# Performance work log

Hardware: AMD Instinct MI355X
Metric: run time of the kernel (lower is better)

Reference implementation:

```python
import jax, jax.numpy as jnp
import numpy as np

B, L, DIN = 2048, 70, 15
HID, NF, K = 16, 4, 40          # hidden_units//2, n_features, kernel_size
C = DIN + 1 + NF                # 20 signature input channels (original + time + conv features)
Z0 = 64
SIG_CH = C + C * C + C ** 3     # 8420, depth-3 signature channels


def setup_inputs() -> dict:
    key = jax.random.key(0)
    ks = jax.random.split(key, 8)
    return {
        "observed_data": jax.random.normal(ks[0], (B, L, DIN), jnp.float32),
        "observed_tp": jnp.linspace(0.0, 1.0, L, dtype=jnp.float32),
        "conv1_w": jax.random.normal(ks[1], (HID, DIN, K), jnp.float32) / np.float32(np.sqrt(DIN * K)),
        "conv1_b": jnp.zeros((HID,), jnp.float32),
        "conv2_w": jax.random.normal(ks[2], (HID, HID), jnp.float32) / np.float32(np.sqrt(HID)),
        "conv2_b": jnp.zeros((HID,), jnp.float32),
        "conv3_w": jax.random.normal(ks[3], (NF, HID), jnp.float32) / np.float32(np.sqrt(HID)),
        "conv3_b": jnp.zeros((NF,), jnp.float32),
        "w_out": jax.random.normal(ks[4], (2 * Z0, SIG_CH), jnp.float32) * np.float32(np.sqrt(2.0 / (SIG_CH + 2 * Z0))),
        "b_out": jnp.zeros((2 * Z0,), jnp.float32),
    }


def _augment(x, w1, b1, w2, b2, w3, b3):
    # x: (B, L, DIN).  signatory.Augment: conv(K) -> relu -> conv1x1 -> relu -> conv1x1,
    # then concat [truncated original, time channel, conv features] along channels.
    xc = jnp.transpose(x, (0, 2, 1))                                   # (B, DIN, L)
    h = jax.lax.conv_general_dilated(xc, w1, (1,), 'VALID')            # (B, HID, Lp)
    h = h + b1[None, :, None]
    h = jnp.einsum('oc,bcl->bol', w2, jax.nn.relu(h)) + b2[None, :, None]
    h = jnp.einsum('oc,bcl->bol', w3, jax.nn.relu(h)) + b3[None, :, None]
    conv_out = jnp.transpose(h, (0, 2, 1))                             # (B, Lp, NF)
    Lp = conv_out.shape[1]
    orig = x[:, K - 1:, :]                                             # (B, Lp, DIN)
    t = jnp.linspace(0.0, 1.0, Lp, dtype=x.dtype)
    time = jnp.broadcast_to(t[None, :, None], (x.shape[0], Lp, 1))
    return jnp.concatenate([orig, time, conv_out], axis=2)             # (B, Lp, C)


def _signature_depth3(path):
    # Truncated (depth 3) path signature with basepoint=True, via Chen's identity:
    # S <- S \otimes exp(dx) over increments, zero basepoint prepended.
    incs = jnp.diff(path, axis=1, prepend=jnp.zeros_like(path[:, :1]))  # (B, Lp, C)
    incs = jnp.transpose(incs, (1, 0, 2))                               # (Lp, B, C)
    Bn, Cn = path.shape[0], path.shape[2]
    s1 = jnp.zeros((Bn, Cn), path.dtype)
    s2 = jnp.zeros((Bn, Cn, Cn), path.dtype)
    s3 = jnp.zeros((Bn, Cn, Cn, Cn), path.dtype)

    def step(carry, d):
        s1, s2, s3 = carry
        e2 = 0.5 * d[:, :, None] * d[:, None, :]                        # d\otimes d / 2
        e3 = (e2[:, :, :, None] * d[:, None, None, :]) / 3.0            # d^{\otimes 3} / 6
        n3 = (s3
              + s2[:, :, :, None] * d[:, None, None, :]
              + s1[:, :, None, None] * e2[:, None, :, :]
              + e3)
        n2 = s2 + s1[:, :, None] * d[:, None, :] + e2
        n1 = s1 + d
        return (n1, n2, n3), None

    (s1, s2, s3), _ = jax.lax.scan(step, (s1, s2, s3), incs)
    return jnp.concatenate([s1, s2.reshape(Bn, -1), s3.reshape(Bn, -1)], axis=1)


def reference(observed_data, observed_tp, conv1_w, conv1_b, conv2_w, conv2_b,
              conv3_w, conv3_b, w_out, b_out):
    # encode_obs_time=False -> observed_tp unused
    path = _augment(observed_data, conv1_w, conv1_b, conv2_w, conv2_b, conv3_w, conv3_b)
    sig = _signature_depth3(path)                                       # (B, SIG_CH)
    z = sig @ w_out.T + b_out                                           # (B, 2*Z0)
    mean_z0 = z[:, :Z0][None]                                           # (1, B, Z0)
    std_z0 = jax.nn.softplus(z[:, Z0:][None])                           # (1, B, Z0)
    return mean_z0, std_z0
```

## Files before the change

kernel.cpp:

```cpp
#include <hip/hip_runtime.h>
#include <math.h>

#define B_TOT 2048
#define D_INC 15
#define KW    40
#define CCH   20
#define LP    31
#define SIGCH 8420
#define SIGP  8448
#define NOUT  128
#define KSPLIT 11
#define KLEN  768

typedef _Float16 f16;
typedef _Float16 f16x8 __attribute__((ext_vector_type(8)));
typedef _Float16 f16x4 __attribute__((ext_vector_type(4)));
typedef _Float16 f16x2 __attribute__((ext_vector_type(2)));
typedef float    f32x4 __attribute__((ext_vector_type(4)));

__global__ __launch_bounds__(256) void k_prep(const float* __restrict__ w1,
                                              f16* __restrict__ wA)
{
    const int ln = threadIdx.x & 63;
    const int wv = threadIdx.x >> 6;
    const int h  = ln & 15;
    const int q4 = ln >> 4;
    for (int gi = 0; gi < 5; ++gi) {
        int g = wv * 5 + gi;
        f16x8 v;
#pragma unroll
        for (int j = 0; j < 8; ++j) {
            int kq = q4 * 8 + j;
            int kk = 2 * g + (kq >> 4);
            int c  = kq & 15;
            v[j] = (c < D_INC) ? (f16)w1[h * 600 + c * 40 + kk] : (f16)0.f;
        }
        *(f16x8*)(wA + g * 512 + ln * 8) = v;
    }
}

__global__ __launch_bounds__(256, 3) void k_augsig(
    const float* __restrict__ x,  const f16* __restrict__ wA, const float* __restrict__ b1,
    const float* __restrict__ w2, const float* __restrict__ b2,
    const float* __restrict__ w3, const float* __restrict__ b3,
    const float* __restrict__ w_out, f16* __restrict__ wh, f16* __restrict__ sig)
{
    if (blockIdx.x >= 512) {
        int t0 = (blockIdx.x - 512) * 256 + threadIdx.x;
        for (int chunk = t0; chunk < 128 * 1056; chunk += 8192) {
            int o  = chunk / 1056;
            int cw = chunk - o * 1056;
            int c0 = cw * 8;
            f16x8 v;
            if (c0 + 8 <= SIGCH) {
                const float* src = w_out + (size_t)o * SIGCH + c0;
                float4 a = *(const float4*)src;
                float4 b = *(const float4*)(src + 4);
                v = (f16x8){(f16)a.x,(f16)a.y,(f16)a.z,(f16)a.w,
                            (f16)b.x,(f16)b.y,(f16)b.z,(f16)b.w};
            } else {
#pragma unroll
                for (int e = 0; e < 8; ++e) {
                    int c = c0 + e;
                    v[e] = (c < SIGCH) ? (f16)w_out[(size_t)o * SIGCH + c] : (f16)0.f;
                }
            }
            *(f16x8*)(wh + (size_t)o * SIGP + c0) = v;
        }
        return;
    }

    __shared__ float pool[12388];
    float* xs    = pool;
    f16*   xp16  = (f16*)(pool + 4272);
    float* h1s   = (float*)xp16;
    float* pprev = pool + 9408;
    float* wsmall= pool + 12032;
    float* w2s = wsmall;        float* b2s = wsmall + 256;
    float* w3s = wsmall + 272;  float* b3s = wsmall + 336;
    float* b1s = wsmall + 340;

    const int tid  = threadIdx.x;
    const int b0   = blockIdx.x * 4;
    const int lane = tid & 63;
    const int w    = tid >> 6;
    const int n16  = lane & 15;
    const int q4   = lane >> 4;

    for (int i = tid; i < 4 * 1050; i += 256) {
        int bl = i / 1050; int t = i - bl * 1050;
        xs[bl * 1068 + t] = x[(size_t)b0 * 1050 + i];
    }
    if (tid < 256) w2s[tid] = w2[tid];
    if (tid < 16)  b2s[tid] = b2[tid];
    if (tid < 64)  w3s[tid] = w3[tid];
    if (tid < 4)   b3s[tid] = b3[tid];
    if (tid < 16)  b1s[tid] = b1[tid];

    f16x8 wa[20];
#pragma unroll
    for (int g = 0; g < 20; ++g) wa[g] = *(const f16x8*)(wA + g * 512 + lane * 8);
    __syncthreads();

    for (int r = tid; r < 280; r += 256) {
        int bl = r / 70; int pos = r - bl * 70;
        const float* src = xs + bl * 1068 + pos * 15;
        f16* dst = xp16 + bl * 1152 + pos * 16;
#pragma unroll
        for (int c = 0; c < 15; ++c) dst[c] = (f16)src[c];
        dst[15] = (f16)0.f;
    }
    __syncthreads();

    f32x4 cacc[2];
#pragma unroll
    for (int tile = 0; tile < 2; ++tile) {
        const int pos0 = tile * 15;
        f32x4 acc = {0.f, 0.f, 0.f, 0.f};
#pragma unroll
        for (int g = 0; g < 20; ++g) {
            const f16x8 bf = *(const f16x8*)&xp16[w * 1152 +
                (pos0 + n16 + 2 * g + (q4 >> 1)) * 16 + (q4 & 1) * 8];
            acc = __builtin_amdgcn_mfma_f32_16x16x32_f16(wa[g], bf, acc, 0, 0, 0);
        }
        cacc[tile] = acc;
    }
    __syncthreads();

#pragma unroll
    for (int tile = 0; tile < 2; ++tile) {
        int pos = tile * 15 + n16;
#pragma unroll
        for (int r = 0; r < 4; ++r) {
            int h = q4 * 4 + r;
            h1s[(w * 31 + pos) * 17 + h] = fmaxf(cacc[tile][r] + b1s[h], 0.f);
        }
    }
    __syncthreads();

    if (tid < 124) {
        const int bl2 = tid / 31;
        const int pos = tid - bl2 * 31;
        float hr[16];
#pragma unroll
        for (int c2 = 0; c2 < 16; ++c2) hr[c2] = h1s[tid * 17 + c2];
        float h2[16];
#pragma unroll
        for (int o = 0; o < 16; ++o) {
            float s = b2s[o];
#pragma unroll
            for (int c2 = 0; c2 < 16; ++c2) s += w2s[o * 16 + c2] * hr[c2];
            h2[o] = fmaxf(s, 0.f);
        }
        float h3[4];
#pragma unroll
        for (int f = 0; f < 4; ++f) {
            float s = b3s[f];
#pragma unroll
            for (int c2 = 0; c2 < 16; ++c2) s += w3s[f * 16 + c2] * h2[c2];
            h3[f] = s;
        }
        float* pr = pprev + bl2 * 656 + 20 + pos * 20;
#pragma unroll
        for (int d = 0; d < D_INC; ++d) pr[d] = xs[bl2 * 1068 + (pos + 39) * 15 + d];
        pr[15] = (float)pos * (1.0f / 30.0f);
#pragma unroll
        for (int f = 0; f < 4; ++f) pr[16 + f] = h3[f];
    } else {
        int z = tid - 124;
        if (z < 80) pprev[(z / 20) * 656 + (z % 20)] = 0.f;
    }
    __syncthreads();

    float* pp   = pprev + w * 656;
    f16*   scr  = (f16*)pool + w * 4704;
    f16*   dtr  = scr;
    f16*   atr  = scr + 800;
    f16*   etr  = scr + 1600;
    f16*   Vb   = scr + 2400;

    for (int e = lane; e < 620; e += 64) {
        int c = e / 31, t = e - c * 31;
        float p0 = pp[t * 20 + c];
        float d  = pp[(t + 1) * 20 + c] - p0;
        dtr[c * 40 + t] = (f16)d;
        atr[c * 40 + t] = (f16)(p0 + 0.5f * d);
        etr[c * 40 + t] = (f16)(0.5f * p0 + d * (1.0f / 6.0f));
    }
    if (lane < 20) {
        dtr[lane * 40 + 31] = (f16)0.f;
        atr[lane * 40 + 31] = (f16)0.f;
        etr[lane * 40 + 31] = (f16)0.f;
    }
    __syncthreads();

    if (lane < 20) {
        f16* vr = Vb + lane * 72;
        float s = 0.f;
        for (int t = 30; t >= 0; --t) {
            float dv = (float)dtr[lane * 40 + t];
            vr[t]      = (f16)s;
            vr[32 + t] = (f16)dv;
            s += dv;
        }
        vr[31] = (f16)0.f;
        vr[63] = (f16)0.f;
    } else if (lane == 20) {
        f16* vr = Vb + 20 * 72;
        for (int k = 0; k < 64; ++k) vr[k] = (k < 31) ? (f16)1.f : (f16)0.f;
    }
    for (int e = lane; e < 11 * 32; e += 64) {
        int row = 21 + (e >> 5);
        int kk  = (e & 31) * 2;
        *(f16x2*)(Vb + row * 72 + kk) = (f16x2){(f16)0.f, (f16)0.f};
    }
    __syncthreads();

    f16x8 bf[2][2];
#pragma unroll
    for (int kc = 0; kc < 2; ++kc)
#pragma unroll
        for (int nt = 0; nt < 2; ++nt)
            bf[kc][nt] = *(const f16x8*)(Vb + (nt * 16 + n16) * 72 + kc * 32 + q4 * 8);

    const int b = b0 + w;
    f16* sg = sig + (size_t)b * SIGP;

    for (int mt = 0; mt < 25; ++mt) {
        const int p = mt * 16 + n16;
        const int i = p / 20, j = p - i * 20;
        f16x8 av = *(const f16x8*)(atr + i * 40 + q4 * 8);
        f16x8 ev = *(const f16x8*)(etr + i * 40 + q4 * 8);
        f16x8 dv = *(const f16x8*)(dtr + j * 40 + q4 * 8);
        f16x8 uf = av * dv;
        f16x8 ef = ev * dv;

        f32x4 a0 = {0.f,0.f,0.f,0.f}, a1 = {0.f,0.f,0.f,0.f};
        a0 = __builtin_amdgcn_mfma_f32_16x16x32_f16(bf[0][0], uf, a0, 0, 0, 0);
        a0 = __builtin_amdgcn_mfma_f32_16x16x32_f16(bf[1][0], ef, a0, 0, 0, 0);
        a1 = __builtin_amdgcn_mfma_f32_16x16x32_f16(bf[0][1], uf, a1, 0, 0, 0);
        a1 = __builtin_amdgcn_mfma_f32_16x16x32_f16(bf[1][1], ef, a1, 0, 0, 0);

        f16x4 s0 = {(f16)a0[0], (f16)a0[1], (f16)a0[2], (f16)a0[3]};
        *(f16x4*)(sg + 420 + p * 20 + q4 * 4) = s0;
        if (q4 == 0) {
            f16x4 s1v = {(f16)a1[0], (f16)a1[1], (f16)a1[2], (f16)a1[3]};
            *(f16x4*)(sg + 420 + p * 20 + 16) = s1v;
        } else if (q4 == 1) {
            sg[20 + p] = (f16)a1[0];
        }
    }

    if (lane < 20) sg[lane] = (f16)pp[620 + lane];
    if (lane < 28) sg[SIGCH + lane] = (f16)0.f;
}

__global__ __launch_bounds__(256) void k_gemm(const f16* __restrict__ sigh,
                                              const f16* __restrict__ wh,
                                              float* __restrict__ z_part)
{
    __shared__ f16 As[2048];
    __shared__ f16 Bs[8192];
    const int tid = threadIdx.x;
    const int l   = tid & 63;
    const int wv  = tid >> 6;
    const int mt  = blockIdx.x / KSPLIT;
    const int s   = blockIdx.x - mt * KSPLIT;
    const int m0  = mt * 32;
    const int kb  = s * KLEN;

    const f32x4 z4 = {0.f, 0.f, 0.f, 0.f};
    f32x4 acc[2][2];
    acc[0][0] = z4; acc[0][1] = z4; acc[1][0] = z4; acc[1][1] = z4;

    const size_t gA = (size_t)(m0 + (tid & 31)) * SIGP + kb + (tid >> 5) * 8;
    size_t gB[4];
#pragma unroll
    for (int r = 0; r < 4; ++r) {
        int slot = r * 256 + tid;
        gB[r] = (size_t)(slot & 127) * SIGP + kb + (slot >> 7) * 8;
    }

    f16x8 aR = *(const f16x8*)(sigh + gA);
    f16x8 bR[4];
#pragma unroll
    for (int r = 0; r < 4; ++r) bR[r] = *(const f16x8*)(wh + gB[r]);

    const int kg   = l >> 4;
    const int mrow = l & 15;

    for (int ch = 0; ch < 12; ++ch) {
        *(f16x8*)&As[tid * 8] = aR;
#pragma unroll
        for (int r = 0; r < 4; ++r) *(f16x8*)&Bs[(r * 256 + tid) * 8] = bR[r];
        __syncthreads();

        if (ch < 11) {
            int koff = (ch + 1) * 64;
            aR = *(const f16x8*)(sigh + gA + koff);
#pragma unroll
            for (int r = 0; r < 4; ++r) bR[r] = *(const f16x8*)(wh + gB[r] + koff);
        }

#pragma unroll
        for (int kc = 0; kc < 2; ++kc) {
            f16x8 aF[2], bF[2];
#pragma unroll
            for (int m2 = 0; m2 < 2; ++m2)
                aF[m2] = *(const f16x8*)&As[((kc * 4 + kg) * 32 + m2 * 16 + mrow) * 8];
#pragma unroll
            for (int n2 = 0; n2 < 2; ++n2)
                bF[n2] = *(const f16x8*)&Bs[((kc * 4 + kg) * 128 + wv * 32 + n2 * 16 + mrow) * 8];
#pragma unroll
            for (int m2 = 0; m2 < 2; ++m2)
#pragma unroll
                for (int n2 = 0; n2 < 2; ++n2)
                    acc[m2][n2] = __builtin_amdgcn_mfma_f32_16x16x32_f16(aF[m2], bF[n2], acc[m2][n2], 0, 0, 0);
        }
        __syncthreads();
    }

#pragma unroll
    for (int m2 = 0; m2 < 2; ++m2) {
#pragma unroll
        for (int n2 = 0; n2 < 2; ++n2) {
            int n = wv * 32 + n2 * 16 + (l & 15);
#pragma unroll
            for (int r = 0; r < 4; ++r) {
                int m = m0 + m2 * 16 + (l >> 4) * 4 + r;
                z_part[((size_t)s * B_TOT + m) * NOUT + n] = acc[m2][n2][r];
            }
        }
    }
}

__global__ __launch_bounds__(256) void k_final(const float* __restrict__ z_part,
                                               const float* __restrict__ b_out,
                                               float* __restrict__ out)
{
    int idx = blockIdx.x * 256 + threadIdx.x;
    int b = idx >> 7;
    int o = idx & 127;
    float z = b_out[o];
#pragma unroll
    for (int s = 0; s < KSPLIT; ++s) z += z_part[((size_t)s * B_TOT + b) * NOUT + o];
    if (o < 64) {
        out[(size_t)b * 64 + o] = z;
    } else {
        float sp = fmaxf(z, 0.f) + log1pf(expf(-fabsf(z)));
        out[131072 + (size_t)b * 64 + (o - 64)] = sp;
    }
}

extern "C" void kernel_launch(void* const* d_in, const int* in_sizes, int n_in,
                              void* d_out, int out_size, void* d_ws, size_t ws_size,
                              hipStream_t stream)
{
    const float* x     = (const float*)d_in[0];
    const float* w1    = (const float*)d_in[2];
    const float* b1    = (const float*)d_in[3];
    const float* w2    = (const float*)d_in[4];
    const float* b2    = (const float*)d_in[5];
    const float* w3    = (const float*)d_in[6];
    const float* b3    = (const float*)d_in[7];
    const float* w_out = (const float*)d_in[8];
    const float* b_out = (const float*)d_in[9];
    float* out = (float*)d_out;

    float* ws    = (float*)d_ws;
    f16*   sigh  = (f16*)ws;
    f16*   wh    = (f16*)(ws + 8650752);
    f16*   wA    = (f16*)(ws + 9191424);
    float* zpart = ws + 9196544;

    hipLaunchKernelGGL(k_prep,   dim3(1),    dim3(256), 0, stream, w1, wA);
    hipLaunchKernelGGL(k_augsig, dim3(544),  dim3(256), 0, stream,
                       x, wA, b1, w2, b2, w3, b3, w_out, wh, sigh);
    hipLaunchKernelGGL(k_gemm,   dim3(704),  dim3(256), 0, stream, sigh, wh, zpart);
    hipLaunchKernelGGL(k_final,  dim3(1024), dim3(256), 0, stream, zpart, b_out, out);
}
```

Baseline: 135.7 us.

## Split augment-signature kernel into one-wave blocks per batch sample

The fused augment and signature kernel now launches one 64-thread block per sample instead of four samples per 256-thread block, with shared memory shrunk to match and the weight-conversion blocks re-indexed. This removes block-wide barriers across four independent waves and lets more small blocks reside per CU, so warps can progress independently. The cost is four times as many blocks, and the small shared weights (w2, w3, biases) are reloaded by each sample.

```diff
diff --git a/kernel.cpp b/kernel.cpp
--- a/kernel.cpp
+++ b/kernel.cpp
@@ -39,14 +39,14 @@
     }
 }
 
-__global__ __launch_bounds__(256, 3) void k_augsig(
+__global__ __launch_bounds__(64, 4) void k_augsig(
     const float* __restrict__ x,  const f16* __restrict__ wA, const float* __restrict__ b1,
     const float* __restrict__ w2, const float* __restrict__ b2,
     const float* __restrict__ w3, const float* __restrict__ b3,
     const float* __restrict__ w_out, f16* __restrict__ wh, f16* __restrict__ sig)
 {
-    if (blockIdx.x >= 512) {
-        int t0 = (blockIdx.x - 512) * 256 + threadIdx.x;
+    if (blockIdx.x >= 2048) {
+        int t0 = (blockIdx.x - 2048) * 64 + threadIdx.x;
         for (int chunk = t0; chunk < 128 * 1056; chunk += 8192) {
             int o  = chunk / 1056;
             int cw = chunk - o * 1056;
@@ -70,42 +70,36 @@
         return;
     }
 
-    __shared__ float pool[12388];
+    __shared__ float pool[3364];
     float* xs    = pool;
-    f16*   xp16  = (f16*)(pool + 4272);
+    f16*   xp16  = (f16*)(pool + 1068);
     float* h1s   = (float*)xp16;
-    float* pprev = pool + 9408;
-    float* wsmall= pool + 12032;
+    float* pprev = pool + 2352;
+    float* wsmall= pool + 3008;
     float* w2s = wsmall;        float* b2s = wsmall + 256;
     float* w3s = wsmall + 272;  float* b3s = wsmall + 336;
     float* b1s = wsmall + 340;
 
-    const int tid  = threadIdx.x;
-    const int b0   = blockIdx.x * 4;
-    const int lane = tid & 63;
-    const int w    = tid >> 6;
+    const int lane = threadIdx.x;
+    const int b    = blockIdx.x;
     const int n16  = lane & 15;
     const int q4   = lane >> 4;
 
-    for (int i = tid; i < 4 * 1050; i += 256) {
-        int bl = i / 1050; int t = i - bl * 1050;
-        xs[bl * 1068 + t] = x[(size_t)b0 * 1050 + i];
-    }
-    if (tid < 256) w2s[tid] = w2[tid];
-    if (tid < 16)  b2s[tid] = b2[tid];
-    if (tid < 64)  w3s[tid] = w3[tid];
-    if (tid < 4)   b3s[tid] = b3[tid];
-    if (tid < 16)  b1s[tid] = b1[tid];
+    for (int i = lane; i < 1050; i += 64) xs[i] = x[(size_t)b * 1050 + i];
+    for (int i = lane; i < 256; i += 64) w2s[i] = w2[i];
+    w3s[lane] = w3[lane];
+    if (lane < 16) b2s[lane] = b2[lane];
+    if (lane < 4)  b3s[lane] = b3[lane];
+    if (lane < 16) b1s[lane] = b1[lane];
 
     f16x8 wa[20];
 #pragma unroll
     for (int g = 0; g < 20; ++g) wa[g] = *(const f16x8*)(wA + g * 512 + lane * 8);
     __syncthreads();
 
-    for (int r = tid; r < 280; r += 256) {
-        int bl = r / 70; int pos = r - bl * 70;
-        const float* src = xs + bl * 1068 + pos * 15;
-        f16* dst = xp16 + bl * 1152 + pos * 16;
+    for (int pos = lane; pos < 70; pos += 64) {
+        const float* src = xs + pos * 15;
+        f16* dst = xp16 + pos * 16;
 #pragma unroll
         for (int c = 0; c < 15; ++c) dst[c] = (f16)src[c];
         dst[15] = (f16)0.f;
@@ -119,7 +113,7 @@
         f32x4 acc = {0.f, 0.f, 0.f, 0.f};
 #pragma unroll
         for (int g = 0; g < 20; ++g) {
-            const f16x8 bf = *(const f16x8*)&xp16[w * 1152 +
+            const f16x8 bf = *(const f16x8*)&xp16[
                 (pos0 + n16 + 2 * g + (q4 >> 1)) * 16 + (q4 & 1) * 8];
             acc = __builtin_amdgcn_mfma_f32_16x16x32_f16(wa[g], bf, acc, 0, 0, 0);
         }
@@ -133,17 +127,16 @@
 #pragma unroll
         for (int r = 0; r < 4; ++r) {
             int h = q4 * 4 + r;
-            h1s[(w * 31 + pos) * 17 + h] = fmaxf(cacc[tile][r] + b1s[h], 0.f);
-        }
-    }
-    __syncthreads();
-
-    if (tid < 124) {
-        const int bl2 = tid / 31;
-        const int pos = tid - bl2 * 31;
+            h1s[pos * 17 + h] = fmaxf(cacc[tile][r] + b1s[h], 0.f);
+        }
+    }
+    __syncthreads();
+
+    if (lane < 31) {
+        const int pos = lane;
         float hr[16];
 #pragma unroll
-        for (int c2 = 0; c2 < 16; ++c2) hr[c2] = h1s[tid * 17 + c2];
+        for (int c2 = 0; c2 < 16; ++c2) hr[c2] = h1s[pos * 17 + c2];
         float h2[16];
 #pragma unroll
         for (int o = 0; o < 16; ++o) {
@@ -160,20 +153,20 @@
             for (int c2 = 0; c2 < 16; ++c2) s += w3s[f * 16 + c2] * h2[c2];
             h3[f] = s;
         }
-        float* pr = pprev + bl2 * 656 + 20 + pos * 20;
-#pragma unroll
-        for (int d = 0; d < D_INC; ++d) pr[d] = xs[bl2 * 1068 + (pos + 39) * 15 + d];
+        float* pr = pprev + 20 + pos * 20;
+#pragma unroll
+        for (int d = 0; d < D_INC; ++d) pr[d] = xs[(pos + 39) * 15 + d];
         pr[15] = (float)pos * (1.0f / 30.0f);
 #pragma unroll
         for (int f = 0; f < 4; ++f) pr[16 + f] = h3[f];
     } else {
-        int z = tid - 124;
-        if (z < 80) pprev[(z / 20) * 656 + (z % 20)] = 0.f;
-    }
-    __syncthreads();
-
-    float* pp   = pprev + w * 656;
-    f16*   scr  = (f16*)pool + w * 4704;
+        int z = lane - 31;
+        if (z < 20) pprev[z] = 0.f;
+    }
+    __syncthreads();
+
+    float* pp   = pprev;
+    f16*   scr  = (f16*)pool;
     f16*   dtr  = scr;
     f16*   atr  = scr + 800;
     f16*   etr  = scr + 1600;
@@ -223,7 +216,6 @@
         for (int nt = 0; nt < 2; ++nt)
             bf[kc][nt] = *(const f16x8*)(Vb + (nt * 16 + n16) * 72 + kc * 32 + q4 * 8);
 
-    const int b = b0 + w;
     f16* sg = sig + (size_t)b * SIGP;
 
     for (int mt = 0; mt < 25; ++mt) {
@@ -374,7 +366,7 @@
     float* zpart = ws + 9196544;
 
     hipLaunchKernelGGL(k_prep,   dim3(1),    dim3(256), 0, stream, w1, wA);
-    hipLaunchKernelGGL(k_augsig, dim3(544),  dim3(256), 0, stream,
+    hipLaunchKernelGGL(k_augsig, dim3(2176), dim3(64),  0, stream,
                        x, wA, b1, w2, b2, w3, b3, w_out, wh, sigh);
     hipLaunchKernelGGL(k_gemm,   dim3(704),  dim3(256), 0, stream, sigh, wh, zpart);
     hipLaunchKernelGGL(k_final,  dim3(1024), dim3(256), 0, stream, zpart, b_out, out);
```

After: 135.8 us. Within noise of the previous version (+0.0%).
